# Performance work log

Measured on AMD Instinct MI355X. Metric: run time of the kernel, lower is better.

## Reference

```python
import jax, jax.numpy as jnp
import numpy as np

B, D_IN, H, C = 8192, 2048, 1024, 1000
LAYERS = [0, 1, 2, 3, 4]          # structure.layers
N_MAIN = 4                        # main hidden layers for layers[1:]
# skip layers in __init__ enumeration order: (target_layer, source_layer)
SKIPS = [(2, 0), (3, 0), (3, 1), (4, 0), (4, 1), (4, 2)]


def _linear_init(key, out_f, in_f):
    k1, k2 = jax.random.split(key)
    bound = 1.0 / np.sqrt(in_f)
    W = jax.random.uniform(k1, (out_f, in_f), minval=-bound, maxval=bound, dtype=jnp.float32)
    b = jax.random.uniform(k2, (out_f,), minval=-bound, maxval=bound, dtype=jnp.float32)
    return W, b


def setup_inputs() -> dict:
    key = jax.random.key(0)
    ks = iter(jax.random.split(key, 40))
    x = jax.random.normal(next(ks), (B, D_IN), dtype=jnp.float32)

    Wf, bf = _linear_init(next(ks), H, D_IN)
    mf = jax.random.bernoulli(next(ks), 0.5, (H, D_IN))

    main_W, main_b, main_m = [], [], []
    for _ in range(N_MAIN):
        W, b = _linear_init(next(ks), H, H)
        main_W.append(W); main_b.append(b)
        main_m.append(jax.random.bernoulli(next(ks), 0.5, (H, H)))

    skip_W, skip_b, skip_m = [], [], []
    for _ in SKIPS:
        W, b = _linear_init(next(ks), H, H)
        skip_W.append(W); skip_b.append(b)
        skip_m.append(jax.random.bernoulli(next(ks), 0.5, (H, H)))

    Wo, bo = _linear_init(next(ks), C, H)
    mo = jax.random.bernoulli(next(ks), 0.5, (C, H))

    return {"x": x, "Wf": Wf, "bf": bf, "mf": mf,
            "main_W": main_W, "main_b": main_b, "main_m": main_m,
            "skip_W": skip_W, "skip_b": skip_b, "skip_m": skip_m,
            "Wo": Wo, "bo": bo, "mo": mo}


def _masked_linear(x, W, b, m):
    # F.linear(x, weight * mask, bias): mask applied to weight before GEMM
    return x @ (W * m).T + b


def reference(x, Wf, bf, mf, main_W, main_b, main_m, skip_W, skip_b, skip_m, Wo, bo, mo):
    relu = jax.nn.relu
    last = relu(_masked_linear(x, Wf, bf, mf))        # layer 0 output, [B, H]
    results = {0: last}
    for i, layer_idx in enumerate(LAYERS[1:]):
        out = relu(_masked_linear(last, main_W[i], main_b[i], main_m[i]))
        for k, (tgt, src) in enumerate(SKIPS):
            if tgt == layer_idx:
                out = out + relu(_masked_linear(results[src], skip_W[k], skip_b[k], skip_m[k]))
        results[layer_idx] = out
        last = out
    return _masked_linear(last, Wo, bo, mo)            # [B, C]
```

## Files before the change

### kernel.cpp

```cpp
#include <hip/hip_runtime.h>
#include <hip/hip_bf16.h>
#include <stdint.h>


typedef unsigned short ushort_t;
typedef __bf16 bf16x8 __attribute__((ext_vector_type(8)));
typedef float f32x4 __attribute__((ext_vector_type(4)));

__device__ __forceinline__ void gl_lds16(const void* g, void* l) {
  typedef __attribute__((address_space(1))) void gvoid;
  typedef __attribute__((address_space(3))) void lvoid;
  __builtin_amdgcn_global_load_lds((gvoid*)(void*)g, (lvoid*)l, 16, 0, 0);
}

__device__ __forceinline__ ushort_t f2b(float f) {
  __hip_bfloat16 h = (__hip_bfloat16)f;
  return *(ushort_t*)&h;
}

__global__ void detect_kernel(const ushort_t* x, const ushort_t* mf, int* flags) {
  __shared__ int s[4];
  if (threadIdx.x < 4) s[threadIdx.x] = 0;
  __syncthreads();
  int expout = 0, m3f80_even = 0, m3f80_odd = 0, mhi01 = 0;
  for (int k = threadIdx.x; k < 2048; k += 256) {
    ushort_t w = x[k];
    int e = (w >> 7) & 0xFF;
    if (e < 96 || e > 144) expout++;
    ushort_t mw = mf[k];
    if (mw == 0x3F80) { if (k & 1) m3f80_odd++; else m3f80_even++; }
    if ((mw >> 8) == 1) mhi01++;
  }
  atomicAdd(&s[0], expout);
  atomicAdd(&s[1], m3f80_even);
  atomicAdd(&s[2], m3f80_odd);
  atomicAdd(&s[3], mhi01);
  __syncthreads();
  if (threadIdx.x == 0) {
    flags[0] = (s[0] > 100) ? 1 : 0;
    int mmode = 0;
    if (s[1] > 100) mmode = 2;
    else if (s[2] > 100) mmode = 3;
    else if (s[3] > 200) mmode = 1;
    flags[1] = mmode;
  }
}

struct PrepEnt {
  const void* w; size_t woff;
  const void* m; size_t moff;
  ushort_t* o;
  int n;
  int valid;
};
struct PrepAll { PrepEnt e[25]; };

__global__ void prep_weights(PrepAll p, const int* flags) {
  const bool f32 = flags[0] != 0;
  const int mmode = flags[1];
  const PrepEnt e = p.e[blockIdx.y];
  const int nch = e.n >> 3;
  const int stride = blockDim.x * gridDim.x;
  for (int ci = blockIdx.x * blockDim.x + threadIdx.x; ci < nch; ci += stride) {
    const int i = ci << 3;
    ushort_t o[8] = {0, 0, 0, 0, 0, 0, 0, 0};
    if (i < e.valid) {
      ushort_t wb[8];
      if (f32) {
        const float* wp = (const float*)e.w + e.woff + i;
        float4 a = *(const float4*)wp;
        float4 b = *(const float4*)(wp + 4);
        wb[0] = f2b(a.x); wb[1] = f2b(a.y); wb[2] = f2b(a.z); wb[3] = f2b(a.w);
        wb[4] = f2b(b.x); wb[5] = f2b(b.y); wb[6] = f2b(b.z); wb[7] = f2b(b.w);
      } else {
        *(uint4*)wb = *(const uint4*)((const ushort_t*)e.w + e.woff + i);
      }
      unsigned mk = 0xFF;
      if (e.m) {
        mk = 0;
        if (mmode == 0) {
          const int4* mp = (const int4*)((const int*)e.m + e.moff + i);
          int4 a = mp[0], b = mp[1];
          mk = (a.x != 0) | ((a.y != 0) << 1) | ((a.z != 0) << 2) | ((a.w != 0) << 3) |
               ((b.x != 0) << 4) | ((b.y != 0) << 5) | ((b.z != 0) << 6) | ((b.w != 0) << 7);
        } else if (mmode == 1) {
          const uint2 mv = *(const uint2*)((const unsigned char*)e.m + e.moff + i);
          const unsigned char* mb = (const unsigned char*)&mv;
          for (int j = 0; j < 8; j++) mk |= (mb[j] != 0) << j;
        } else if (mmode == 2) {
          uint4 mv = *(const uint4*)((const ushort_t*)e.m + e.moff + i);
          const ushort_t* ms = (const ushort_t*)&mv;
          for (int j = 0; j < 8; j++) mk |= (ms[j] != 0) << j;
        } else {
          const uint4* mp = (const uint4*)((const unsigned int*)e.m + e.moff + i);
          uint4 a = mp[0], b = mp[1];
          const unsigned* u = (const unsigned*)&a;
          const unsigned* v = (const unsigned*)&b;
          for (int j = 0; j < 4; j++) mk |= (u[j] != 0) << j;
          for (int j = 0; j < 4; j++) mk |= (v[j] != 0) << (4 + j);
        }
      }
#pragma unroll
      for (int j = 0; j < 8; j++) o[j] = ((mk >> j) & 1) ? wb[j] : (ushort_t)0;
    }
    *(uint4*)(e.o + i) = *(uint4*)o;
  }
}

struct GemmSrc { const ushort_t* A; const ushort_t* B; const ushort_t* bias; };
struct GemmArgs { GemmSrc s[4]; };

#define SBAR()  asm volatile("s_barrier" ::: "memory")
#define LGKM0() asm volatile("s_waitcnt lgkmcnt(0)" ::: "memory")
#define VMC8()  asm volatile("s_waitcnt vmcnt(8)" ::: "memory")
#define VMC0()  asm volatile("s_waitcnt vmcnt(0)" ::: "memory")

template <int NSRC, bool RELU, bool NGUARD>
__launch_bounds__(256, 2)
__global__ void gemm_multi(GemmArgs args, void* Cv, const int* of32flag,
                           int K, int N_real, int ldc)
{
  __shared__ __align__(16) ushort_t lds[2][16384];

  const bool of32 = (of32flag != nullptr) && (of32flag[0] != 0);
  __hip_bfloat16* C = (__hip_bfloat16*)Cv;
  float* Cf = (float*)Cv;

  const int tid  = threadIdx.x;
  const int lane = tid & 63;
  const int wave = tid >> 6;
  const int wm = (wave >> 1) * 64;
  const int wn = (wave & 1) * 64;
  const int fr = lane & 15;
  const int kg = lane >> 4;

  const int lid = blockIdx.x;
  const int xcd = lid & 7, chunk = lid >> 3;
  const int bm = (xcd * 8 + (chunk >> 3)) * 128;
  const int bn = (chunk & 7) * 128;

  const int rbase = tid >> 3;
  const int sg    = (tid & 7) ^ (rbase & 7);
  const size_t aoff = (size_t)(bm + rbase) * K + sg * 8;
  const size_t boff = (size_t)(bn + rbase) * K + sg * 8;
  const size_t rs32 = (size_t)32 * K;

  auto stage = [&](const ushort_t* gA, const ushort_t* gB, int buf) {
    ushort_t* base = &lds[buf][0];
    ushort_t* lA = base + wave * 512;
    ushort_t* lB = base + 8192 + wave * 512;
    gl_lds16(gA,            lA);
    gl_lds16(gA + rs32,     lA + 2048);
    gl_lds16(gA + 2 * rs32, lA + 4096);
    gl_lds16(gA + 3 * rs32, lA + 6144);
    gl_lds16(gB,            lB);
    gl_lds16(gB + rs32,     lB + 2048);
    gl_lds16(gB + 2 * rs32, lB + 4096);
    gl_lds16(gB + 3 * rs32, lB + 6144);
  };

  const int s0   = (kg ^ (fr & 7)) * 16;
  const int arow = (wm + fr) * 128;
  const int brow = 16384 + (wn + fr) * 128;

  f32x4 acc[4][4], out_acc[4][4];
#pragma unroll
  for (int i = 0; i < 4; i++)
#pragma unroll
    for (int j = 0; j < 4; j++) {
      acc[i][j] = (f32x4){0.f, 0.f, 0.f, 0.f};
      if (NSRC > 1) out_acc[i][j] = (f32x4){0.f, 0.f, 0.f, 0.f};
    }

  float bpre[NSRC][4];
#pragma unroll
  for (int s = 0; s < NSRC; ++s)
#pragma unroll
    for (int ni = 0; ni < 4; ni++)
      bpre[s][ni] = (float)*(const __hip_bfloat16*)
          (args.s[s].bias + bn + wn + ni * 16 + fr);

  const int TPS = K >> 6;
  const int NT  = TPS * NSRC;

  bf16x8 af0[4], bf0[4], af1[4], bf1[4];

  auto rdfrag0 = [&](const char* Lb, int ks) {
    const int so = s0 ^ (ks * 64);
#pragma unroll
    for (int m = 0; m < 4; ++m) af0[m] = *(const bf16x8*)(Lb + arow + m * 2048 + so);
#pragma unroll
    for (int n = 0; n < 4; ++n) bf0[n] = *(const bf16x8*)(Lb + brow + n * 2048 + so);
  };
  auto rdfrag1 = [&](const char* Lb, int ks) {
    const int so = s0 ^ (ks * 64);
#pragma unroll
    for (int m = 0; m < 4; ++m) af1[m] = *(const bf16x8*)(Lb + arow + m * 2048 + so);
#pragma unroll
    for (int n = 0; n < 4; ++n) bf1[n] = *(const bf16x8*)(Lb + brow + n * 2048 + so);
  };
  auto mfma16_0 = [&]() {
    __builtin_amdgcn_s_setprio(1);
#pragma unroll
    for (int mi = 0; mi < 4; mi++)
#pragma unroll
      for (int ni = 0; ni < 4; ni++)
        acc[mi][ni] = __builtin_amdgcn_mfma_f32_16x16x32_bf16(
            af0[mi], bf0[ni], acc[mi][ni], 0, 0, 0);
    __builtin_amdgcn_s_setprio(0);
  };
  auto mfma16_1 = [&]() {
    __builtin_amdgcn_s_setprio(1);
#pragma unroll
    for (int mi = 0; mi < 4; mi++)
#pragma unroll
      for (int ni = 0; ni < 4; ni++)
        acc[mi][ni] = __builtin_amdgcn_mfma_f32_16x16x32_bf16(
            af1[mi], bf1[ni], acc[mi][ni], 0, 0, 0);
    __builtin_amdgcn_s_setprio(0);
  };

  stage(args.s[0].A + aoff, args.s[0].B + boff, 0);
  {
    const int s1 = 1 / TPS, k1 = (1 % TPS) * 64;
    stage(args.s[s1].A + aoff + k1, args.s[s1].B + boff + k1, 1);
  }
  VMC8();
  SBAR();
  rdfrag0((const char*)&lds[0][0], 0);

  int psrc = 2 / TPS, pk0 = (2 % TPS) * 64;
  int csrc = 0, ck = 0;
  int cur = 0;

  for (int t = 0; t < NT; ++t) {
    const char* Lb = (const char*)&lds[cur][0];

    rdfrag1(Lb, 1);
    __builtin_amdgcn_sched_barrier(0);
    mfma16_0();

    LGKM0();
    SBAR();

    ck += 64;
    const bool srcEnd = (ck == K);
    const bool more2 = (t + 2 < NT);
    if (more2) {
      stage(args.s[psrc].A + aoff + pk0, args.s[psrc].B + boff + pk0, cur);
      pk0 += 64; if (pk0 == K) { pk0 = 0; ++psrc; }
    }

    if (t + 1 < NT) {
      if (more2) VMC8(); else VMC0();
      SBAR();
      rdfrag0((const char*)&lds[cur ^ 1][0], 0);
    }
    __builtin_amdgcn_sched_barrier(0);
    mfma16_1();

    if (NSRC > 1 && srcEnd) {
      float bb[4];
#pragma unroll
      for (int s = 0; s < NSRC; ++s)
        if (s == csrc) {
#pragma unroll
          for (int ni = 0; ni < 4; ni++) bb[ni] = bpre[s][ni];
        }
#pragma unroll
      for (int ni = 0; ni < 4; ni++)
#pragma unroll
        for (int mi = 0; mi < 4; mi++)
#pragma unroll
          for (int j = 0; j < 4; j++) {
            float v = acc[mi][ni][j] + bb[ni];
            if (RELU) v = fmaxf(v, 0.0f);
            out_acc[mi][ni][j] += v;
            acc[mi][ni][j] = 0.0f;
          }
      ck = 0; ++csrc;
    }

    cur ^= 1;
  }

#pragma unroll
  for (int ni = 0; ni < 4; ni++) {
    const int c = bn + wn + ni * 16 + fr;
    if (NGUARD && c >= N_real) continue;
#pragma unroll
    for (int mi = 0; mi < 4; mi++) {
      const int r0 = bm + wm + mi * 16 + kg * 4;
#pragma unroll
      for (int j = 0; j < 4; j++) {
        const size_t idx = (size_t)(r0 + j) * ldc + c;
        float v;
        if (NSRC == 1) {
          v = acc[mi][ni][j] + bpre[0][ni];
          if (RELU) v = fmaxf(v, 0.0f);
        } else {
          v = out_acc[mi][ni][j];
        }
        if (of32) Cf[idx] = v;
        else      C[idx]  = (__hip_bfloat16)v;
      }
    }
  }
}

extern "C" void kernel_launch(void* const* d_in, const int* in_sizes, int n_in,
                              void* d_out, int out_size, void* d_ws, size_t ws_size,
                              hipStream_t stream) {
  (void)out_size; (void)ws_size;
  const int Bm = 8192, DIN = 2048, H = 1024, Cn = 1000;
  const size_t HH = (size_t)H * H;

  struct PO { const void* p; size_t off; };
  PO x{d_in[0], 0}, Wf{d_in[0], 0}, mf{d_in[0], 0}, Wo{d_in[0], 0}, mo{d_in[0], 0};
  PO bf{d_in[0], 0}, bo{d_in[0], 0};
  PO mW[4], mM[4], mB[4], sW[6], sM[6], sB[6];
  for (int i = 0; i < 4; i++) { mW[i] = {d_in[0], 0}; mM[i] = mW[i]; mB[i] = mW[i]; }
  for (int i = 0; i < 6; i++) { sW[i] = {d_in[0], 0}; sM[i] = sW[i]; sB[i] = sW[i]; }

  {
    int c2M = 0, c1M = 0, c1k = 0, cWoMo = 0, c4 = 0, c6 = 0;
    for (int i = 0; i < n_in; i++) {
      const int s = in_sizes[i];
      const void* p = d_in[i];
      switch (s) {
        case 16777216: x = {p, 0}; break;
        case 2097152:  if (c2M++ == 0) Wf = {p, 0}; else mf = {p, 0}; break;
        case 1048576: {
          int j = c1M++;
          if (j < 4)       mW[j]      = {p, 0};
          else if (j < 8)  mM[j - 4]  = {p, 0};
          else if (j < 14) sW[j - 8]  = {p, 0};
          else if (j < 20) sM[j - 14] = {p, 0};
          break;
        }
        case 1024: {
          int j = c1k++;
          if (j == 0)      bf        = {p, 0};
          else if (j < 5)  mB[j - 1] = {p, 0};
          else if (j < 11) sB[j - 5] = {p, 0};
          break;
        }
        case 1024000: if (cWoMo++ == 0) Wo = {p, 0}; else mo = {p, 0}; break;
        case 1000: bo = {p, 0}; break;
        case 4194304:
          for (int t = 0; t < 4; t++) {
            if (c4 == 0) mW[t] = {p, t * HH}; else mM[t] = {p, t * HH};
          }
          c4++; break;
        case 6291456:
          for (int t = 0; t < 6; t++) {
            if (c6 == 0) sW[t] = {p, t * HH}; else sM[t] = {p, t * HH};
          }
          c6++; break;
        case 4096:
          for (int t = 0; t < 4; t++) mB[t] = {p, (size_t)t * H};
          break;
        case 6144:
          for (int t = 0; t < 6; t++) sB[t] = {p, (size_t)t * H};
          break;
        default: break;
      }
    }
  }

  ushort_t* wsp = (ushort_t*)d_ws;
  size_t off = 0;
  int* flags = (int*)wsp; off += 32;
  ushort_t* xc = wsp + off; off += (size_t)Bm * DIN;
  __hip_bfloat16* r[5];
  for (int i = 0; i < 5; i++) { r[i] = (__hip_bfloat16*)(wsp + off); off += (size_t)Bm * H; }
  ushort_t* wWf = wsp + off; off += (size_t)H * DIN;
  ushort_t* wMain[4];
  for (int i = 0; i < 4; i++) { wMain[i] = wsp + off; off += HH; }
  ushort_t* wSkip[6];
  for (int k = 0; k < 6; k++) { wSkip[k] = wsp + off; off += HH; }
  ushort_t* wWo = wsp + off; off += (size_t)1024 * 1024;
  ushort_t* cbf_ = wsp + off; off += 1024;
  ushort_t* cmB[4];
  for (int i = 0; i < 4; i++) { cmB[i] = wsp + off; off += 1024; }
  ushort_t* csB[6];
  for (int k = 0; k < 6; k++) { csB[k] = wsp + off; off += 1024; }
  ushort_t* cbo = wsp + off; off += 1024;

  detect_kernel<<<1, 256, 0, stream>>>((const ushort_t*)x.p, (const ushort_t*)mf.p, flags);

  PrepAll p;
  p.e[0]  = { Wf.p, Wf.off, mf.p, mf.off, wWf, H * DIN, H * DIN };
  for (int i = 0; i < 4; i++)
    p.e[1 + i] = { mW[i].p, mW[i].off, mM[i].p, mM[i].off, wMain[i], (int)HH, (int)HH };
  for (int k = 0; k < 6; k++)
    p.e[5 + k] = { sW[k].p, sW[k].off, sM[k].p, sM[k].off, wSkip[k], (int)HH, (int)HH };
  p.e[11] = { Wo.p, Wo.off, mo.p, mo.off, wWo, 1024 * 1024, Cn * H };
  p.e[12] = { bf.p, bf.off, nullptr, 0, cbf_, H, H };
  for (int i = 0; i < 4; i++)
    p.e[13 + i] = { mB[i].p, mB[i].off, nullptr, 0, cmB[i], H, H };
  for (int k = 0; k < 6; k++)
    p.e[17 + k] = { sB[k].p, sB[k].off, nullptr, 0, csB[k], H, H };
  p.e[23] = { bo.p, bo.off, nullptr, 0, cbo, 1024, Cn };
  p.e[24] = { x.p, x.off, nullptr, 0, xc, Bm * DIN, Bm * DIN };
  prep_weights<<<dim3(256, 25), dim3(256), 0, stream>>>(p, flags);

  const dim3 g(512), b(256);

  GemmArgs a0; a0.s[0] = { xc, wWf, cbf_ };
  gemm_multi<1, true, false><<<g, b, 0, stream>>>(a0, r[0], nullptr, DIN, H, H);

  GemmArgs a1; a1.s[0] = { (ushort_t*)r[0], wMain[0], cmB[0] };
  gemm_multi<1, true, false><<<g, b, 0, stream>>>(a1, r[1], nullptr, H, H, H);

  GemmArgs a2;
  a2.s[0] = { (ushort_t*)r[1], wMain[1], cmB[1] };
  a2.s[1] = { (ushort_t*)r[0], wSkip[0], csB[0] };
  gemm_multi<2, true, false><<<g, b, 0, stream>>>(a2, r[2], nullptr, H, H, H);

  GemmArgs a3;
  a3.s[0] = { (ushort_t*)r[2], wMain[2], cmB[2] };
  a3.s[1] = { (ushort_t*)r[0], wSkip[1], csB[1] };
  a3.s[2] = { (ushort_t*)r[1], wSkip[2], csB[2] };
  gemm_multi<3, true, false><<<g, b, 0, stream>>>(a3, r[3], nullptr, H, H, H);

  GemmArgs a4;
  a4.s[0] = { (ushort_t*)r[3], wMain[3], cmB[3] };
  a4.s[1] = { (ushort_t*)r[0], wSkip[3], csB[3] };
  a4.s[2] = { (ushort_t*)r[1], wSkip[4], csB[4] };
  a4.s[3] = { (ushort_t*)r[2], wSkip[5], csB[5] };
  gemm_multi<4, true, false><<<g, b, 0, stream>>>(a4, r[4], nullptr, H, H, H);

  GemmArgs ao; ao.s[0] = { (ushort_t*)r[4], wWo, cbo };
  gemm_multi<1, false, true><<<g, b, 0, stream>>>(ao, d_out, flags, H, Cn, Cn);
}
```

Baseline: 515.8 us.

## Replace LDS-staged GEMM pipeline with direct global-to-register fragment loads

Removes the shared-memory double buffer, async global-to-LDS copies, and barriers from the multi-source GEMM. Each wave now loads its bf16x8 MFMA fragments directly from global memory into two register buffers, alternating over 32-wide K steps. This is meant to remove barrier and LDS read overhead and to free LDS for occupancy. The cost is that tiles are no longer shared across waves, so global/L2 traffic rises and the loads use an uncoalesced strided pattern.

```diff
diff --git a/kernel.cpp b/kernel.cpp
--- a/kernel.cpp
+++ b/kernel.cpp
@@ -6,12 +6,6 @@
 typedef unsigned short ushort_t;
 typedef __bf16 bf16x8 __attribute__((ext_vector_type(8)));
 typedef float f32x4 __attribute__((ext_vector_type(4)));
-
-__device__ __forceinline__ void gl_lds16(const void* g, void* l) {
-  typedef __attribute__((address_space(1))) void gvoid;
-  typedef __attribute__((address_space(3))) void lvoid;
-  __builtin_amdgcn_global_load_lds((gvoid*)(void*)g, (lvoid*)l, 16, 0, 0);
-}
 
 __device__ __forceinline__ ushort_t f2b(float f) {
   __hip_bfloat16 h = (__hip_bfloat16)f;
@@ -110,18 +104,11 @@
 struct GemmSrc { const ushort_t* A; const ushort_t* B; const ushort_t* bias; };
 struct GemmArgs { GemmSrc s[4]; };
 
-#define SBAR()  asm volatile("s_barrier" ::: "memory")
-#define LGKM0() asm volatile("s_waitcnt lgkmcnt(0)" ::: "memory")
-#define VMC8()  asm volatile("s_waitcnt vmcnt(8)" ::: "memory")
-#define VMC0()  asm volatile("s_waitcnt vmcnt(0)" ::: "memory")
-
 template <int NSRC, bool RELU, bool NGUARD>
 __launch_bounds__(256, 2)
 __global__ void gemm_multi(GemmArgs args, void* Cv, const int* of32flag,
                            int K, int N_real, int ldc)
 {
-  __shared__ __align__(16) ushort_t lds[2][16384];
-
   const bool of32 = (of32flag != nullptr) && (of32flag[0] != 0);
   __hip_bfloat16* C = (__hip_bfloat16*)Cv;
   float* Cf = (float*)Cv;
@@ -139,29 +126,12 @@
   const int bm = (xcd * 8 + (chunk >> 3)) * 128;
   const int bn = (chunk & 7) * 128;
 
-  const int rbase = tid >> 3;
-  const int sg    = (tid & 7) ^ (rbase & 7);
-  const size_t aoff = (size_t)(bm + rbase) * K + sg * 8;
-  const size_t boff = (size_t)(bn + rbase) * K + sg * 8;
-  const size_t rs32 = (size_t)32 * K;
-
-  auto stage = [&](const ushort_t* gA, const ushort_t* gB, int buf) {
-    ushort_t* base = &lds[buf][0];
-    ushort_t* lA = base + wave * 512;
-    ushort_t* lB = base + 8192 + wave * 512;
-    gl_lds16(gA,            lA);
-    gl_lds16(gA + rs32,     lA + 2048);
-    gl_lds16(gA + 2 * rs32, lA + 4096);
-    gl_lds16(gA + 3 * rs32, lA + 6144);
-    gl_lds16(gB,            lB);
-    gl_lds16(gB + rs32,     lB + 2048);
-    gl_lds16(gB + 2 * rs32, lB + 4096);
-    gl_lds16(gB + 3 * rs32, lB + 6144);
-  };
-
-  const int s0   = (kg ^ (fr & 7)) * 16;
-  const int arow = (wm + fr) * 128;
-  const int brow = 16384 + (wn + fr) * 128;
+  uint32_t avo[4], bvo[4];
+#pragma unroll
+  for (int i = 0; i < 4; ++i) {
+    avo[i] = (uint32_t)(bm + wm + i * 16 + fr) * (uint32_t)K + (uint32_t)(kg * 8);
+    bvo[i] = (uint32_t)(bn + wn + i * 16 + fr) * (uint32_t)K + (uint32_t)(kg * 8);
+  }
 
   f32x4 acc[4][4], out_acc[4][4];
 #pragma unroll
@@ -180,24 +150,37 @@
       bpre[s][ni] = (float)*(const __hip_bfloat16*)
           (args.s[s].bias + bn + wn + ni * 16 + fr);
 
-  const int TPS = K >> 6;
-  const int NT  = TPS * NSRC;
-
-  bf16x8 af0[4], bf0[4], af1[4], bf1[4];
-
-  auto rdfrag0 = [&](const char* Lb, int ks) {
-    const int so = s0 ^ (ks * 64);
-#pragma unroll
-    for (int m = 0; m < 4; ++m) af0[m] = *(const bf16x8*)(Lb + arow + m * 2048 + so);
-#pragma unroll
-    for (int n = 0; n < 4; ++n) bf0[n] = *(const bf16x8*)(Lb + brow + n * 2048 + so);
-  };
-  auto rdfrag1 = [&](const char* Lb, int ks) {
-    const int so = s0 ^ (ks * 64);
-#pragma unroll
-    for (int m = 0; m < 4; ++m) af1[m] = *(const bf16x8*)(Lb + arow + m * 2048 + so);
-#pragma unroll
-    for (int n = 0; n < 4; ++n) bf1[n] = *(const bf16x8*)(Lb + brow + n * 2048 + so);
+  const int K32 = K >> 5;
+  const int NS  = K32 * NSRC;
+
+  bf16x8 a0[4], b0[4], a1[4], b1[4];
+
+  const ushort_t* As = args.s[0].A;
+  const ushort_t* Bs = args.s[0].B;
+  int pk = 0, ps = 0;
+
+  auto advance = [&]() {
+    pk += 32;
+    if (pk == K) {
+      pk = 0; ++ps;
+      if (NSRC > 1 && ps < NSRC) { As = args.s[ps].A; Bs = args.s[ps].B; }
+    }
+  };
+  auto load0 = [&]() {
+    const ushort_t* pa = As + pk;
+    const ushort_t* pb = Bs + pk;
+#pragma unroll
+    for (int i = 0; i < 4; ++i) a0[i] = *(const bf16x8*)(pa + avo[i]);
+#pragma unroll
+    for (int i = 0; i < 4; ++i) b0[i] = *(const bf16x8*)(pb + bvo[i]);
+  };
+  auto load1 = [&]() {
+    const ushort_t* pa = As + pk;
+    const ushort_t* pb = Bs + pk;
+#pragma unroll
+    for (int i = 0; i < 4; ++i) a1[i] = *(const bf16x8*)(pa + avo[i]);
+#pragma unroll
+    for (int i = 0; i < 4; ++i) b1[i] = *(const bf16x8*)(pb + bvo[i]);
   };
   auto mfma16_0 = [&]() {
     __builtin_amdgcn_s_setprio(1);
@@ -206,7 +189,7 @@
 #pragma unroll
       for (int ni = 0; ni < 4; ni++)
         acc[mi][ni] = __builtin_amdgcn_mfma_f32_16x16x32_bf16(
-            af0[mi], bf0[ni], acc[mi][ni], 0, 0, 0);
+            a0[mi], b0[ni], acc[mi][ni], 0, 0, 0);
     __builtin_amdgcn_s_setprio(0);
   };
   auto mfma16_1 = [&]() {
@@ -216,50 +199,24 @@
 #pragma unroll
       for (int ni = 0; ni < 4; ni++)
         acc[mi][ni] = __builtin_amdgcn_mfma_f32_16x16x32_bf16(
-            af1[mi], bf1[ni], acc[mi][ni], 0, 0, 0);
+            a1[mi], b1[ni], acc[mi][ni], 0, 0, 0);
     __builtin_amdgcn_s_setprio(0);
   };
 
-  stage(args.s[0].A + aoff, args.s[0].B + boff, 0);
-  {
-    const int s1 = 1 / TPS, k1 = (1 % TPS) * 64;
-    stage(args.s[s1].A + aoff + k1, args.s[s1].B + boff + k1, 1);
-  }
-  VMC8();
-  SBAR();
-  rdfrag0((const char*)&lds[0][0], 0);
-
-  int psrc = 2 / TPS, pk0 = (2 % TPS) * 64;
+  load0(); advance();
+  load1(); advance();
+
   int csrc = 0, ck = 0;
-  int cur = 0;
-
-  for (int t = 0; t < NT; ++t) {
-    const char* Lb = (const char*)&lds[cur][0];
-
-    rdfrag1(Lb, 1);
-    __builtin_amdgcn_sched_barrier(0);
+
+  for (int u = 0; u < NS; u += 2) {
     mfma16_0();
-
-    LGKM0();
-    SBAR();
+    if (u + 2 < NS) { load0(); advance(); }
+
+    mfma16_1();
+    if (u + 3 < NS) { load1(); advance(); }
 
     ck += 64;
-    const bool srcEnd = (ck == K);
-    const bool more2 = (t + 2 < NT);
-    if (more2) {
-      stage(args.s[psrc].A + aoff + pk0, args.s[psrc].B + boff + pk0, cur);
-      pk0 += 64; if (pk0 == K) { pk0 = 0; ++psrc; }
-    }
-
-    if (t + 1 < NT) {
-      if (more2) VMC8(); else VMC0();
-      SBAR();
-      rdfrag0((const char*)&lds[cur ^ 1][0], 0);
-    }
-    __builtin_amdgcn_sched_barrier(0);
-    mfma16_1();
-
-    if (NSRC > 1 && srcEnd) {
+    if (NSRC > 1 && ck == K) {
       float bb[4];
 #pragma unroll
       for (int s = 0; s < NSRC; ++s)
@@ -280,8 +237,6 @@
           }
       ck = 0; ++csrc;
     }
-
-    cur ^= 1;
   }
 
 #pragma unroll
```

Measured after the change: 995.7 us. +93.0%, slower.

## Fuse detect, prep and all GEMM layers into one persistent kernel with grid barriers

Applied to the files above, without the earlier changes.

Replaces the eight separate launches (format detection, weight prep, six GEMM layers) with a single persistent kernel of 512 blocks that synchronises through atomic grid-wide barriers in workspace memory. The GEMM body turns from compile-time templated NSRC/RELU/NGUARD into runtime parameters. The aim is to remove per-launch overhead and the tail gaps between kernels. The risks are weaker code generation from runtime branching and extra registers (out_acc and bpre[4][4] are always allocated). The barriers also assume all 512 blocks are co-resident, and a memset is added to reset the barrier counters.

```diff
diff --git a/kernel.cpp b/kernel.cpp
--- a/kernel.cpp
+++ b/kernel.cpp
@@ -6,6 +6,11 @@
 typedef unsigned short ushort_t;
 typedef __bf16 bf16x8 __attribute__((ext_vector_type(8)));
 typedef float f32x4 __attribute__((ext_vector_type(4)));
+
+#define SBAR()  asm volatile("s_barrier" ::: "memory")
+#define LGKM0() asm volatile("s_waitcnt lgkmcnt(0)" ::: "memory")
+#define VMC8()  asm volatile("s_waitcnt vmcnt(8)" ::: "memory")
+#define VMC0()  asm volatile("s_waitcnt vmcnt(0)" ::: "memory")
 
 __device__ __forceinline__ void gl_lds16(const void* g, void* l) {
   typedef __attribute__((address_space(1))) void gvoid;
@@ -18,111 +23,46 @@
   return *(ushort_t*)&h;
 }
 
-__global__ void detect_kernel(const ushort_t* x, const ushort_t* mf, int* flags) {
-  __shared__ int s[4];
-  if (threadIdx.x < 4) s[threadIdx.x] = 0;
-  __syncthreads();
-  int expout = 0, m3f80_even = 0, m3f80_odd = 0, mhi01 = 0;
-  for (int k = threadIdx.x; k < 2048; k += 256) {
-    ushort_t w = x[k];
-    int e = (w >> 7) & 0xFF;
-    if (e < 96 || e > 144) expout++;
-    ushort_t mw = mf[k];
-    if (mw == 0x3F80) { if (k & 1) m3f80_odd++; else m3f80_even++; }
-    if ((mw >> 8) == 1) mhi01++;
-  }
-  atomicAdd(&s[0], expout);
-  atomicAdd(&s[1], m3f80_even);
-  atomicAdd(&s[2], m3f80_odd);
-  atomicAdd(&s[3], mhi01);
+__device__ __forceinline__ void gbar(int* bar, int p) {
+  __threadfence();
   __syncthreads();
   if (threadIdx.x == 0) {
-    flags[0] = (s[0] > 100) ? 1 : 0;
-    int mmode = 0;
-    if (s[1] > 100) mmode = 2;
-    else if (s[2] > 100) mmode = 3;
-    else if (s[3] > 200) mmode = 1;
-    flags[1] = mmode;
-  }
+    __hip_atomic_fetch_add(bar + p, 1, __ATOMIC_ACQ_REL, __HIP_MEMORY_SCOPE_AGENT);
+    while (__hip_atomic_load(bar + p, __ATOMIC_ACQUIRE, __HIP_MEMORY_SCOPE_AGENT)
+           < (int)gridDim.x)
+      __builtin_amdgcn_s_sleep(2);
+  }
+  __syncthreads();
+  __threadfence();
 }
 
 struct PrepEnt {
-  const void* w; size_t woff;
-  const void* m; size_t moff;
+  const void* w;
+  const void* m;
   ushort_t* o;
+  int woff;
+  int moff;
   int n;
   int valid;
 };
-struct PrepAll { PrepEnt e[25]; };
-
-__global__ void prep_weights(PrepAll p, const int* flags) {
-  const bool f32 = flags[0] != 0;
-  const int mmode = flags[1];
-  const PrepEnt e = p.e[blockIdx.y];
-  const int nch = e.n >> 3;
-  const int stride = blockDim.x * gridDim.x;
-  for (int ci = blockIdx.x * blockDim.x + threadIdx.x; ci < nch; ci += stride) {
-    const int i = ci << 3;
-    ushort_t o[8] = {0, 0, 0, 0, 0, 0, 0, 0};
-    if (i < e.valid) {
-      ushort_t wb[8];
-      if (f32) {
-        const float* wp = (const float*)e.w + e.woff + i;
-        float4 a = *(const float4*)wp;
-        float4 b = *(const float4*)(wp + 4);
-        wb[0] = f2b(a.x); wb[1] = f2b(a.y); wb[2] = f2b(a.z); wb[3] = f2b(a.w);
-        wb[4] = f2b(b.x); wb[5] = f2b(b.y); wb[6] = f2b(b.z); wb[7] = f2b(b.w);
-      } else {
-        *(uint4*)wb = *(const uint4*)((const ushort_t*)e.w + e.woff + i);
-      }
-      unsigned mk = 0xFF;
-      if (e.m) {
-        mk = 0;
-        if (mmode == 0) {
-          const int4* mp = (const int4*)((const int*)e.m + e.moff + i);
-          int4 a = mp[0], b = mp[1];
-          mk = (a.x != 0) | ((a.y != 0) << 1) | ((a.z != 0) << 2) | ((a.w != 0) << 3) |
-               ((b.x != 0) << 4) | ((b.y != 0) << 5) | ((b.z != 0) << 6) | ((b.w != 0) << 7);
-        } else if (mmode == 1) {
-          const uint2 mv = *(const uint2*)((const unsigned char*)e.m + e.moff + i);
-          const unsigned char* mb = (const unsigned char*)&mv;
-          for (int j = 0; j < 8; j++) mk |= (mb[j] != 0) << j;
-        } else if (mmode == 2) {
-          uint4 mv = *(const uint4*)((const ushort_t*)e.m + e.moff + i);
-          const ushort_t* ms = (const ushort_t*)&mv;
-          for (int j = 0; j < 8; j++) mk |= (ms[j] != 0) << j;
-        } else {
-          const uint4* mp = (const uint4*)((const unsigned int*)e.m + e.moff + i);
-          uint4 a = mp[0], b = mp[1];
-          const unsigned* u = (const unsigned*)&a;
-          const unsigned* v = (const unsigned*)&b;
-          for (int j = 0; j < 4; j++) mk |= (u[j] != 0) << j;
-          for (int j = 0; j < 4; j++) mk |= (v[j] != 0) << (4 + j);
-        }
-      }
-#pragma unroll
-      for (int j = 0; j < 8; j++) o[j] = ((mk >> j) & 1) ? wb[j] : (ushort_t)0;
-    }
-    *(uint4*)(e.o + i) = *(uint4*)o;
-  }
-}
-
-struct GemmSrc { const ushort_t* A; const ushort_t* B; const ushort_t* bias; };
-struct GemmArgs { GemmSrc s[4]; };
-
-#define SBAR()  asm volatile("s_barrier" ::: "memory")
-#define LGKM0() asm volatile("s_waitcnt lgkmcnt(0)" ::: "memory")
-#define VMC8()  asm volatile("s_waitcnt vmcnt(8)" ::: "memory")
-#define VMC0()  asm volatile("s_waitcnt vmcnt(0)" ::: "memory")
-
-template <int NSRC, bool RELU, bool NGUARD>
-__launch_bounds__(256, 2)
-__global__ void gemm_multi(GemmArgs args, void* Cv, const int* of32flag,
-                           int K, int N_real, int ldc)
+
+struct MegaArgs {
+  PrepEnt pe[25];
+  const ushort_t* Ap[6][4];
+  const ushort_t* Bp[6][4];
+  const ushort_t* bp[6][4];
+  void* Cp[6];
+  int* flags;
+  int* bar;
+};
+
+__device__ __forceinline__ void gemm_layer(
+    const ushort_t* const Asrc[4], const ushort_t* const Bsrc[4],
+    const ushort_t* const bsrc[4], void* Cv,
+    const int nsrc, const int K, const int N_real, const int ldc,
+    const bool RELU, const bool NGUARD, const bool of32,
+    ushort_t (&lds)[2][16384])
 {
-  __shared__ __align__(16) ushort_t lds[2][16384];
-
-  const bool of32 = (of32flag != nullptr) && (of32flag[0] != 0);
   __hip_bfloat16* C = (__hip_bfloat16*)Cv;
   float* Cf = (float*)Cv;
 
@@ -169,19 +109,20 @@
 #pragma unroll
     for (int j = 0; j < 4; j++) {
       acc[i][j] = (f32x4){0.f, 0.f, 0.f, 0.f};
-      if (NSRC > 1) out_acc[i][j] = (f32x4){0.f, 0.f, 0.f, 0.f};
-    }
-
-  float bpre[NSRC][4];
-#pragma unroll
-  for (int s = 0; s < NSRC; ++s)
+      out_acc[i][j] = (f32x4){0.f, 0.f, 0.f, 0.f};
+    }
+
+  float bpre[4][4];
+#pragma unroll
+  for (int s = 0; s < 4; ++s)
 #pragma unroll
     for (int ni = 0; ni < 4; ni++)
-      bpre[s][ni] = (float)*(const __hip_bfloat16*)
-          (args.s[s].bias + bn + wn + ni * 16 + fr);
+      bpre[s][ni] = (s < nsrc)
+          ? (float)*(const __hip_bfloat16*)(bsrc[s] + bn + wn + ni * 16 + fr)
+          : 0.0f;
 
   const int TPS = K >> 6;
-  const int NT  = TPS * NSRC;
+  const int NT  = TPS * nsrc;
 
   bf16x8 af0[4], bf0[4], af1[4], bf1[4];
 
@@ -220,16 +161,13 @@
     __builtin_amdgcn_s_setprio(0);
   };
 
-  stage(args.s[0].A + aoff, args.s[0].B + boff, 0);
-  {
-    const int s1 = 1 / TPS, k1 = (1 % TPS) * 64;
-    stage(args.s[s1].A + aoff + k1, args.s[s1].B + boff + k1, 1);
-  }
+  stage(Asrc[0] + aoff, Bsrc[0] + boff, 0);
+  stage(Asrc[0] + aoff + 64, Bsrc[0] + boff + 64, 1);
   VMC8();
   SBAR();
   rdfrag0((const char*)&lds[0][0], 0);
 
-  int psrc = 2 / TPS, pk0 = (2 % TPS) * 64;
+  int psrc = 0, pk0 = 128;
   int csrc = 0, ck = 0;
   int cur = 0;
 
@@ -247,7 +185,7 @@
     const bool srcEnd = (ck == K);
     const bool more2 = (t + 2 < NT);
     if (more2) {
-      stage(args.s[psrc].A + aoff + pk0, args.s[psrc].B + boff + pk0, cur);
+      stage(Asrc[psrc] + aoff + pk0, Bsrc[psrc] + boff + pk0, cur);
       pk0 += 64; if (pk0 == K) { pk0 = 0; ++psrc; }
     }
 
@@ -259,10 +197,10 @@
     __builtin_amdgcn_sched_barrier(0);
     mfma16_1();
 
-    if (NSRC > 1 && srcEnd) {
+    if (nsrc > 1 && srcEnd) {
       float bb[4];
 #pragma unroll
-      for (int s = 0; s < NSRC; ++s)
+      for (int s = 0; s < 4; ++s)
         if (s == csrc) {
 #pragma unroll
           for (int ni = 0; ni < 4; ni++) bb[ni] = bpre[s][ni];
@@ -295,7 +233,7 @@
       for (int j = 0; j < 4; j++) {
         const size_t idx = (size_t)(r0 + j) * ldc + c;
         float v;
-        if (NSRC == 1) {
+        if (nsrc == 1) {
           v = acc[mi][ni][j] + bpre[0][ni];
           if (RELU) v = fmaxf(v, 0.0f);
         } else {
@@ -305,6 +243,111 @@
         else      C[idx]  = (__hip_bfloat16)v;
       }
     }
+  }
+}
+
+__global__ __launch_bounds__(256, 2) void meganet(MegaArgs ma) {
+  __shared__ __align__(16) ushort_t lds[2][16384];
+  const int tid = threadIdx.x;
+  int* flags = ma.flags;
+  int* bar = ma.bar;
+
+  if (blockIdx.x == 0) {
+    int* sdet = (int*)&lds[0][0];
+    if (tid < 4) sdet[tid] = 0;
+    __syncthreads();
+    const ushort_t* x  = (const ushort_t*)ma.pe[24].w;
+    const ushort_t* mf = (const ushort_t*)ma.pe[0].m;
+    int expout = 0, m3f80_even = 0, m3f80_odd = 0, mhi01 = 0;
+    for (int k = tid; k < 2048; k += 256) {
+      ushort_t w = x[k];
+      int e = (w >> 7) & 0xFF;
+      if (e < 96 || e > 144) expout++;
+      ushort_t mw = mf[k];
+      if (mw == 0x3F80) { if (k & 1) m3f80_odd++; else m3f80_even++; }
+      if ((mw >> 8) == 1) mhi01++;
+    }
+    atomicAdd(&sdet[0], expout);
+    atomicAdd(&sdet[1], m3f80_even);
+    atomicAdd(&sdet[2], m3f80_odd);
+    atomicAdd(&sdet[3], mhi01);
+    __syncthreads();
+    if (tid == 0) {
+      flags[0] = (sdet[0] > 100) ? 1 : 0;
+      int mmode = 0;
+      if (sdet[1] > 100) mmode = 2;
+      else if (sdet[2] > 100) mmode = 3;
+      else if (sdet[3] > 200) mmode = 1;
+      flags[1] = mmode;
+    }
+  }
+  gbar(bar, 0);
+
+  {
+    const bool f32 = flags[0] != 0;
+    const int mmode = flags[1];
+    const int stride = gridDim.x * blockDim.x;
+    for (int ei = 0; ei < 25; ++ei) {
+      const PrepEnt e = ma.pe[ei];
+      const int nch = e.n >> 3;
+      for (int ci = blockIdx.x * blockDim.x + tid; ci < nch; ci += stride) {
+        const int i = ci << 3;
+        ushort_t o[8] = {0, 0, 0, 0, 0, 0, 0, 0};
+        if (i < e.valid) {
+          ushort_t wb[8];
+          if (f32) {
+            const float* wp = (const float*)e.w + e.woff + i;
+            float4 a = *(const float4*)wp;
+            float4 b = *(const float4*)(wp + 4);
+            wb[0] = f2b(a.x); wb[1] = f2b(a.y); wb[2] = f2b(a.z); wb[3] = f2b(a.w);
+            wb[4] = f2b(b.x); wb[5] = f2b(b.y); wb[6] = f2b(b.z); wb[7] = f2b(b.w);
+          } else {
+            *(uint4*)wb = *(const uint4*)((const ushort_t*)e.w + e.woff + i);
+          }
+          unsigned mk = 0xFF;
+          if (e.m) {
+            mk = 0;
+            if (mmode == 0) {
+              const int4* mp = (const int4*)((const int*)e.m + e.moff + i);
+              int4 a = mp[0], b = mp[1];
+              mk = (a.x != 0) | ((a.y != 0) << 1) | ((a.z != 0) << 2) | ((a.w != 0) << 3) |
+                   ((b.x != 0) << 4) | ((b.y != 0) << 5) | ((b.z != 0) << 6) | ((b.w != 0) << 7);
+            } else if (mmode == 1) {
+              const uint2 mv = *(const uint2*)((const unsigned char*)e.m + e.moff + i);
+              const unsigned char* mb = (const unsigned char*)&mv;
+              for (int j = 0; j < 8; j++) mk |= (mb[j] != 0) << j;
+            } else if (mmode == 2) {
+              uint4 mv = *(const uint4*)((const ushort_t*)e.m + e.moff + i);
+              const ushort_t* ms = (const ushort_t*)&mv;
+              for (int j = 0; j < 8; j++) mk |= (ms[j] != 0) << j;
+            } else {
+              const uint4* mp = (const uint4*)((const unsigned int*)e.m + e.moff + i);
+              uint4 a = mp[0], b = mp[1];
+              const unsigned* u = (const unsigned*)&a;
+              const unsigned* v = (const unsigned*)&b;
+              for (int j = 0; j < 4; j++) mk |= (u[j] != 0) << j;
+              for (int j = 0; j < 4; j++) mk |= (v[j] != 0) << (4 + j);
+            }
+          }
+#pragma unroll
+          for (int j = 0; j < 8; j++) o[j] = ((mk >> j) & 1) ? wb[j] : (ushort_t)0;
+        }
+        *(uint4*)(e.o + i) = *(uint4*)o;
+      }
+    }
+  }
+  gbar(bar, 1);
+
+  for (int li = 0; li < 6; ++li) {
+    const bool last = (li == 5);
+    int nsrc = 1;
+    if (li >= 2 && li <= 4) nsrc = li;
+    const int K = (li == 0) ? 2048 : 1024;
+    const bool of32 = last && (flags[0] != 0);
+    gemm_layer(ma.Ap[li], ma.Bp[li], ma.bp[li], ma.Cp[li],
+               nsrc, K, last ? 1000 : 1024, last ? 1000 : 1024,
+               !last, last, of32, lds);
+    if (li < 5) gbar(bar, 2 + li);
   }
 }
 
@@ -370,7 +413,8 @@
 
   ushort_t* wsp = (ushort_t*)d_ws;
   size_t off = 0;
-  int* flags = (int*)wsp; off += 32;
+  int* bar = (int*)wsp; off += 64;
+  int* flags = (int*)(wsp + off); off += 32;
   ushort_t* xc = wsp + off; off += (size_t)Bm * DIN;
   __hip_bfloat16* r[5];
   for (int i = 0; i < 5; i++) { r[i] = (__hip_bfloat16*)(wsp + off); off += (size_t)Bm * H; }
@@ -387,50 +431,42 @@
   for (int k = 0; k < 6; k++) { csB[k] = wsp + off; off += 1024; }
   ushort_t* cbo = wsp + off; off += 1024;
 
-  detect_kernel<<<1, 256, 0, stream>>>((const ushort_t*)x.p, (const ushort_t*)mf.p, flags);
-
-  PrepAll p;
-  p.e[0]  = { Wf.p, Wf.off, mf.p, mf.off, wWf, H * DIN, H * DIN };
+  MegaArgs ma;
+  ma.flags = flags;
+  ma.bar = bar;
+  ma.pe[0]  = { Wf.p, mf.p, wWf, (int)Wf.off, (int)mf.off, H * DIN, H * DIN };
   for (int i = 0; i < 4; i++)
-    p.e[1 + i] = { mW[i].p, mW[i].off, mM[i].p, mM[i].off, wMain[i], (int)HH, (int)HH };
+    ma.pe[1 + i] = { mW[i].p, mM[i].p, wMain[i], (int)mW[i].off, (int)mM[i].off, (int)HH, (int)HH };
   for (int k = 0; k < 6; k++)
-    p.e[5 + k] = { sW[k].p, sW[k].off, sM[k].p, sM[k].off, wSkip[k], (int)HH, (int)HH };
-  p.e[11] = { Wo.p, Wo.off, mo.p, mo.off, wWo, 1024 * 1024, Cn * H };
-  p.e[12] = { bf.p, bf.off, nullptr, 0, cbf_, H, H };
+    ma.pe[5 + k] = { sW[k].p, sM[k].p, wSkip[k], (int)sW[k].off, (int)sM[k].off, (int)HH, (int)HH };
+  ma.pe[11] = { Wo.p, mo.p, wWo, (int)Wo.off, (int)mo.off, 1024 * 1024, Cn * H };
+  ma.pe[12] = { bf.p, nullptr, cbf_, (int)bf.off, 0, H, H };
   for (int i = 0; i < 4; i++)
-    p.e[13 + i] = { mB[i].p, mB[i].off, nullptr, 0, cmB[i], H, H };
+    ma.pe[13 + i] = { mB[i].p, nullptr, cmB[i], (int)mB[i].off, 0, H, H };
   for (int k = 0; k < 6; k++)
-    p.e[17 + k] = { sB[k].p, sB[k].off, nullptr, 0, csB[k], H, H };
-  p.e[23] = { bo.p, bo.off, nullptr, 0, cbo, 1024, Cn };
-  p.e[24] = { x.p, x.off, nullptr, 0, xc, Bm * DIN, Bm * DIN };
-  prep_weights<<<dim3(256, 25), dim3(256), 0, stream>>>(p, flags);
-
-  const dim3 g(512), b(256);
-
-  GemmArgs a0; a0.s[0] = { xc, wWf, cbf_ };
-  gemm_multi<1, true, false><<<g, b, 0, stream>>>(a0, r[0], nullptr, DIN, H, H);
-
-  GemmArgs a1; a1.s[0] = { (ushort_t*)r[0], wMain[0], cmB[0] };
-  gemm_multi<1, true, false><<<g, b, 0, stream>>>(a1, r[1], nullptr, H, H, H);
-
-  GemmArgs a2;
-  a2.s[0] = { (ushort_t*)r[1], wMain[1], cmB[1] };
-  a2.s[1] = { (ushort_t*)r[0], wSkip[0], csB[0] };
-  gemm_multi<2, true, false><<<g, b, 0, stream>>>(a2, r[2], nullptr, H, H, H);
-
-  GemmArgs a3;
-  a3.s[0] = { (ushort_t*)r[2], wMain[2], cmB[2] };
-  a3.s[1] = { (ushort_t*)r[0], wSkip[1], csB[1] };
-  a3.s[2] = { (ushort_t*)r[1], wSkip[2], csB[2] };
-  gemm_multi<3, true, false><<<g, b, 0, stream>>>(a3, r[3], nullptr, H, H, H);
-
-  GemmArgs a4;
-  a4.s[0] = { (ushort_t*)r[3], wMain[3], cmB[3] };
-  a4.s[1] = { (ushort_t*)r[0], wSkip[3], csB[3] };
-  a4.s[2] = { (ushort_t*)r[1], wSkip[4], csB[4] };
-  a4.s[3] = { (ushort_t*)r[2], wSkip[5], csB[5] };
-  gemm_multi<4, true, false><<<g, b, 0, stream>>>(a4, r[4], nullptr, H, H, H);
-
-  GemmArgs ao; ao.s[0] = { (ushort_t*)r[4], wWo, cbo };
-  gemm_multi<1, false, true><<<g, b, 0, stream>>>(ao, d_out, flags, H, Cn, Cn);
-}
+    ma.pe[17 + k] = { sB[k].p, nullptr, csB[k], (int)sB[k].off, 0, H, H };
+  ma.pe[23] = { bo.p, nullptr, cbo, (int)bo.off, 0, 1024, Cn };
+  ma.pe[24] = { x.p, nullptr, xc, (int)x.off, 0, Bm * DIN, Bm * DIN };
+
+  for (int li = 0; li < 6; ++li)
+    for (int s = 0; s < 4; ++s) { ma.Ap[li][s] = xc; ma.Bp[li][s] = wWf; ma.bp[li][s] = cbf_; }
+
+  ma.Ap[0][0] = xc;                 ma.Bp[0][0] = wWf;      ma.bp[0][0] = cbf_;
+  ma.Ap[1][0] = (ushort_t*)r[0];    ma.Bp[1][0] = wMain[0]; ma.bp[1][0] = cmB[0];
+  ma.Ap[2][0] = (ushort_t*)r[1];    ma.Bp[2][0] = wMain[1]; ma.bp[2][0] = cmB[1];
+  ma.Ap[2][1] = (ushort_t*)r[0];    ma.Bp[2][1] = wSkip[0]; ma.bp[2][1] = csB[0];
+  ma.Ap[3][0] = (ushort_t*)r[2];    ma.Bp[3][0] = wMain[2]; ma.bp[3][0] = cmB[2];
+  ma.Ap[3][1] = (ushort_t*)r[0];    ma.Bp[3][1] = wSkip[1]; ma.bp[3][1] = csB[1];
+  ma.Ap[3][2] = (ushort_t*)r[1];    ma.Bp[3][2] = wSkip[2]; ma.bp[3][2] = csB[2];
+  ma.Ap[4][0] = (ushort_t*)r[3];    ma.Bp[4][0] = wMain[3]; ma.bp[4][0] = cmB[3];
+  ma.Ap[4][1] = (ushort_t*)r[0];    ma.Bp[4][1] = wSkip[3]; ma.bp[4][1] = csB[3];
+  ma.Ap[4][2] = (ushort_t*)r[1];    ma.Bp[4][2] = wSkip[4]; ma.bp[4][2] = csB[4];
+  ma.Ap[4][3] = (ushort_t*)r[2];    ma.Bp[4][3] = wSkip[5]; ma.bp[4][3] = csB[5];
+  ma.Ap[5][0] = (ushort_t*)r[4];    ma.Bp[5][0] = wWo;      ma.bp[5][0] = cbo;
+
+  ma.Cp[0] = r[0]; ma.Cp[1] = r[1]; ma.Cp[2] = r[2];
+  ma.Cp[3] = r[3]; ma.Cp[4] = r[4]; ma.Cp[5] = d_out;
+
+  hipMemsetAsync(d_ws, 0, 128, stream);
+  meganet<<<dim3(512), dim3(256), 0, stream>>>(ma);
+}
```

Result: slower. 1.839 ms (+256.5%).

## Load GEMM B operand directly from global into registers, bypassing LDS

Applied to the files above, without the earlier changes.

The B (weight) tile is no longer staged through shared memory. Each lane now reads its B fragments straight from global memory into registers, while only the A tile stays double-buffered in LDS, so the LDS footprint is halved. The aim is to cut LDS traffic and barrier pressure for B. In exchange, B reads from global are less coalesced and are no longer shared between waves, and their latency is only partly hidden because they are consumed shortly after being issued.

```diff
diff --git a/kernel.cpp b/kernel.cpp
--- a/kernel.cpp
+++ b/kernel.cpp
@@ -113,6 +113,7 @@
 #define SBAR()  asm volatile("s_barrier" ::: "memory")
 #define LGKM0() asm volatile("s_waitcnt lgkmcnt(0)" ::: "memory")
 #define VMC8()  asm volatile("s_waitcnt vmcnt(8)" ::: "memory")
+#define VMC4()  asm volatile("s_waitcnt vmcnt(4)" ::: "memory")
 #define VMC0()  asm volatile("s_waitcnt vmcnt(0)" ::: "memory")
 
 template <int NSRC, bool RELU, bool NGUARD>
@@ -120,7 +121,7 @@
 __global__ void gemm_multi(GemmArgs args, void* Cv, const int* of32flag,
                            int K, int N_real, int ldc)
 {
-  __shared__ __align__(16) ushort_t lds[2][16384];
+  __shared__ __align__(16) ushort_t lds[2][8192];
 
   const bool of32 = (of32flag != nullptr) && (of32flag[0] != 0);
   __hip_bfloat16* C = (__hip_bfloat16*)Cv;
@@ -142,26 +143,23 @@
   const int rbase = tid >> 3;
   const int sg    = (tid & 7) ^ (rbase & 7);
   const size_t aoff = (size_t)(bm + rbase) * K + sg * 8;
-  const size_t boff = (size_t)(bn + rbase) * K + sg * 8;
   const size_t rs32 = (size_t)32 * K;
 
-  auto stage = [&](const ushort_t* gA, const ushort_t* gB, int buf) {
-    ushort_t* base = &lds[buf][0];
-    ushort_t* lA = base + wave * 512;
-    ushort_t* lB = base + 8192 + wave * 512;
+  auto stageA = [&](const ushort_t* gA, int buf) {
+    ushort_t* lA = &lds[buf][0] + wave * 512;
     gl_lds16(gA,            lA);
     gl_lds16(gA + rs32,     lA + 2048);
     gl_lds16(gA + 2 * rs32, lA + 4096);
     gl_lds16(gA + 3 * rs32, lA + 6144);
-    gl_lds16(gB,            lB);
-    gl_lds16(gB + rs32,     lB + 2048);
-    gl_lds16(gB + 2 * rs32, lB + 4096);
-    gl_lds16(gB + 3 * rs32, lB + 6144);
   };
 
   const int s0   = (kg ^ (fr & 7)) * 16;
   const int arow = (wm + fr) * 128;
-  const int brow = 16384 + (wn + fr) * 128;
+
+  size_t bro[4];
+#pragma unroll
+  for (int n = 0; n < 4; ++n)
+    bro[n] = (size_t)(bn + wn + n * 16 + fr) * (size_t)K + (size_t)(kg * 8);
 
   f32x4 acc[4][4], out_acc[4][4];
 #pragma unroll
@@ -185,19 +183,25 @@
 
   bf16x8 af0[4], bf0[4], af1[4], bf1[4];
 
-  auto rdfrag0 = [&](const char* Lb, int ks) {
+  auto rdA0 = [&](const char* Lb, int ks) {
     const int so = s0 ^ (ks * 64);
 #pragma unroll
     for (int m = 0; m < 4; ++m) af0[m] = *(const bf16x8*)(Lb + arow + m * 2048 + so);
-#pragma unroll
-    for (int n = 0; n < 4; ++n) bf0[n] = *(const bf16x8*)(Lb + brow + n * 2048 + so);
-  };
-  auto rdfrag1 = [&](const char* Lb, int ks) {
+  };
+  auto rdA1 = [&](const char* Lb, int ks) {
     const int so = s0 ^ (ks * 64);
 #pragma unroll
     for (int m = 0; m < 4; ++m) af1[m] = *(const bf16x8*)(Lb + arow + m * 2048 + so);
-#pragma unroll
-    for (int n = 0; n < 4; ++n) bf1[n] = *(const bf16x8*)(Lb + brow + n * 2048 + so);
+  };
+  auto rdB0 = [&](const ushort_t* Bk, int ks) {
+    const ushort_t* p = Bk + ks * 32;
+#pragma unroll
+    for (int n = 0; n < 4; ++n) bf0[n] = *(const bf16x8*)(p + bro[n]);
+  };
+  auto rdB1 = [&](const ushort_t* Bk, int ks) {
+    const ushort_t* p = Bk + ks * 32;
+#pragma unroll
+    for (int n = 0; n < 4; ++n) bf1[n] = *(const bf16x8*)(p + bro[n]);
   };
   auto mfma16_0 = [&]() {
     __builtin_amdgcn_s_setprio(1);
@@ -220,14 +224,17 @@
     __builtin_amdgcn_s_setprio(0);
   };
 
-  stage(args.s[0].A + aoff, args.s[0].B + boff, 0);
+  stageA(args.s[0].A + aoff, 0);
   {
     const int s1 = 1 / TPS, k1 = (1 % TPS) * 64;
-    stage(args.s[s1].A + aoff + k1, args.s[s1].B + boff + k1, 1);
-  }
-  VMC8();
+    stageA(args.s[s1].A + aoff + k1, 1);
+  }
+  VMC4();
   SBAR();
-  rdfrag0((const char*)&lds[0][0], 0);
+  const ushort_t* Bt = args.s[0].B;
+  int btk = 0, bsV = 0;
+  rdA0((const char*)&lds[0][0], 0);
+  rdB0(Bt + btk, 0);
 
   int psrc = 2 / TPS, pk0 = (2 % TPS) * 64;
   int csrc = 0, ck = 0;
@@ -236,7 +243,8 @@
   for (int t = 0; t < NT; ++t) {
     const char* Lb = (const char*)&lds[cur][0];
 
-    rdfrag1(Lb, 1);
+    rdA1(Lb, 1);
+    rdB1(Bt + btk, 1);
     __builtin_amdgcn_sched_barrier(0);
     mfma16_0();
 
@@ -247,14 +255,16 @@
     const bool srcEnd = (ck == K);
     const bool more2 = (t + 2 < NT);
     if (more2) {
-      stage(args.s[psrc].A + aoff + pk0, args.s[psrc].B + boff + pk0, cur);
+      stageA(args.s[psrc].A + aoff + pk0, cur);
       pk0 += 64; if (pk0 == K) { pk0 = 0; ++psrc; }
     }
 
     if (t + 1 < NT) {
       if (more2) VMC8(); else VMC0();
       SBAR();
-      rdfrag0((const char*)&lds[cur ^ 1][0], 0);
+      btk += 64; if (btk == K) { btk = 0; ++bsV; Bt = args.s[bsV].B; }
+      rdA0((const char*)&lds[cur ^ 1][0], 0);
+      rdB0(Bt + btk, 0);
     }
     __builtin_amdgcn_sched_barrier(0);
     mfma16_1();
```

Result: slower. 714.4 us (+38.5%).
